# Kernel optimization log

Measured on AMD Instinct MI355X. Metric: run time of the kernel, lower is better.

Reference implementation:

```python
import jax, jax.numpy as jnp
import numpy as np

B, S, H, C = 2, 128, 768, 5
NEG = -1024.0

def setup_inputs() -> dict:
    key = jax.random.key(0)
    ks = jax.random.split(key, 6)
    sequence_output = jax.random.normal(ks[0], (B, S, H), dtype=jnp.float32)
    attention_mask = jnp.ones((B, S), dtype=jnp.int32)
    ng_token_mask = jax.random.bernoulli(ks[1], 0.5, (B, S, C, S))  # bool
    target = (jax.random.uniform(ks[2], (B, S, C, S)) < 0.01).astype(jnp.float32)
    lim = 1.0 / np.sqrt(H)
    W_prd = jax.random.uniform(ks[3], (H, H), jnp.float32, -lim, lim)
    b_prd = jnp.zeros((H,), jnp.float32)
    W_arg = jax.random.uniform(ks[4], (C * H, H), jnp.float32, -lim, lim)
    b_arg = jnp.zeros((C * H,), jnp.float32)
    W_out = jax.random.uniform(ks[5], (C, H), jnp.float32, -lim, lim)
    return dict(sequence_output=sequence_output, attention_mask=attention_mask,
                ng_token_mask=ng_token_mask, target=target,
                W_prd=W_prd, b_prd=b_prd, W_arg=W_arg, b_arg=b_arg, W_out=W_out)

def reference(sequence_output, attention_mask, ng_token_mask, target,
              W_prd, b_prd, W_arg, b_arg, W_out):
    b, s, h = sequence_output.shape
    c = W_out.shape[0]
    # get_mask: ng mask restricted to attended tokens, then any over case dim
    mask = ng_token_mask & (attention_mask[:, None, None, :] > 0)   # (B,S,C,S)
    mask = jnp.any(mask, axis=2, keepdims=True)                      # (B,S,1,S)
    # dropout is identity in eval mode
    h_p = sequence_output @ W_prd.T + b_prd                          # (B,S,H)
    h_a = (sequence_output @ W_arg.T + b_arg).reshape(b, s, c, h)    # (B,S,C,H)
    # outer-sum biaffine: (B, S_prd, S_arg, C, H)
    hh = jnp.tanh(h_p[:, :, None, None, :] + h_a[:, None, :, :, :])
    # per-case Linear(H,1,bias=False), stacked at dim=2 -> (B, S_prd, C, S_arg)
    output = jnp.einsum('bpach,ch->bpca', hh, W_out)
    output = output + (~mask).astype(output.dtype) * NEG
    # cross_entropy_pas_loss: multi-hot CE over candidate (last) axis
    log_sm = jax.nn.log_softmax(output, axis=3)
    loss = jnp.sum(-log_sm * target) / jnp.sum(target)
    return loss, output
```

## Files before the change

### kernel.cpp

```cpp
#include <hip/hip_runtime.h>
#include <math.h>

#define Bb 2
#define Ss 128
#define Hh 768
#define Cc 5
#define Mm 256
#define NEGV -1024.0f
#define SCALE 2.8853900817779268f

#define PT 2
#define NBLK (Mm / PT * Cc)
#define NBUCKET 32

typedef __attribute__((ext_vector_type(8))) short bf16x8;
typedef __attribute__((ext_vector_type(4))) float f32x4;
typedef unsigned short ushort;

__device__ __forceinline__ unsigned pack_hi16(float hi, float lo) {
    return (__float_as_uint(hi) & 0xFFFF0000u) | (__float_as_uint(lo) >> 16);
}
__device__ __forceinline__ bf16x8 pack_bf16x8(float4 lo, float4 hi) {
    union { bf16x8 v; unsigned u[4]; } r;
    r.u[0] = pack_hi16(lo.y, lo.x);
    r.u[1] = pack_hi16(lo.w, lo.z);
    r.u[2] = pack_hi16(hi.y, hi.x);
    r.u[3] = pack_hi16(hi.w, hi.z);
    return r.v;
}
__device__ __forceinline__ ushort bf16_rne(float f) {
    unsigned b = __float_as_uint(f);
    return (ushort)((b + 0x7FFFu + ((b >> 16) & 1u)) >> 16);
}

#define SB __builtin_amdgcn_sched_barrier(0);

__global__ __launch_bounds__(256)
void gemm_mfma(const float* __restrict__ X,
               const float* __restrict__ Wprd,
               const float* __restrict__ Warg,
               const float* __restrict__ bprd,
               const float* __restrict__ barg,
               float* __restrict__ EpG,
               ushort* __restrict__ haTb,
               float* __restrict__ accumArr)
{
    __shared__ __align__(16) ushort Asb[64][72];
    __shared__ __align__(16) ushort Bsb[32][72];

    if (blockIdx.x == 0 && blockIdx.y == 0) {
        for (int i = threadIdx.x; i < NBUCKET * 32; i += 256) accumArr[i] = 0.f;
    }
    const int bm   = blockIdx.x;
    const int bn   = blockIdx.y;
    const int tid  = threadIdx.x;
    const int wave = tid >> 6;
    const int lane = tid & 63;
    const int l16  = lane & 15;
    const int quad = lane >> 4;

    const float* Wsrc; const float* bsrc;
    const int nb = bn * 32;
    if (nb < Hh) { Wsrc = Wprd + (size_t)nb * Hh;        bsrc = bprd + nb; }
    else         { Wsrc = Warg + (size_t)(nb - Hh) * Hh; bsrc = barg + (nb - Hh); }

    const int srow = tid >> 2;
    const int sko  = (tid & 3) * 8;
    const float* gA = X + (size_t)(bm * 64 + srow) * Hh + sko;
    const float* gB = Wsrc + (size_t)(tid >> 2) * Hh + sko;

    float4 a00 = *(const float4*)(gA);
    float4 a01 = *(const float4*)(gA + 4);
    float4 a10 = *(const float4*)(gA + 32);
    float4 a11 = *(const float4*)(gA + 36);
    float4 b00, b01, b10, b11;
    if (tid < 128) {
        b00 = *(const float4*)(gB);      b01 = *(const float4*)(gB + 4);
        b10 = *(const float4*)(gB + 32); b11 = *(const float4*)(gB + 36);
    }

    f32x4 acc0 = {0.f,0.f,0.f,0.f}, acc1 = {0.f,0.f,0.f,0.f};

    for (int k0 = 0; k0 < Hh; k0 += 64) {
        *(bf16x8*)&Asb[srow][sko]      = pack_bf16x8(a00, a01);
        *(bf16x8*)&Asb[srow][sko + 32] = pack_bf16x8(a10, a11);
        if (tid < 128) {
            *(bf16x8*)&Bsb[tid >> 2][sko]      = pack_bf16x8(b00, b01);
            *(bf16x8*)&Bsb[tid >> 2][sko + 32] = pack_bf16x8(b10, b11);
        }
        __syncthreads();
        if (k0 + 64 < Hh) {
            a00 = *(const float4*)(gA + k0 + 64);
            a01 = *(const float4*)(gA + k0 + 68);
            a10 = *(const float4*)(gA + k0 + 96);
            a11 = *(const float4*)(gA + k0 + 100);
            if (tid < 128) {
                b00 = *(const float4*)(gB + k0 + 64);
                b01 = *(const float4*)(gB + k0 + 68);
                b10 = *(const float4*)(gB + k0 + 96);
                b11 = *(const float4*)(gB + k0 + 100);
            }
        }
        {
            bf16x8 af0 = *(const bf16x8*)&Asb[wave * 16 + l16][quad * 8];
            bf16x8 c00 = *(const bf16x8*)&Bsb[l16][quad * 8];
            bf16x8 c10 = *(const bf16x8*)&Bsb[16 + l16][quad * 8];
            acc0 = __builtin_amdgcn_mfma_f32_16x16x32_bf16(af0, c00, acc0, 0, 0, 0);
            acc1 = __builtin_amdgcn_mfma_f32_16x16x32_bf16(af0, c10, acc1, 0, 0, 0);
            bf16x8 af1 = *(const bf16x8*)&Asb[wave * 16 + l16][quad * 8 + 32];
            bf16x8 c01 = *(const bf16x8*)&Bsb[l16][quad * 8 + 32];
            bf16x8 c11 = *(const bf16x8*)&Bsb[16 + l16][quad * 8 + 32];
            acc0 = __builtin_amdgcn_mfma_f32_16x16x32_bf16(af1, c01, acc0, 0, 0, 0);
            acc1 = __builtin_amdgcn_mfma_f32_16x16x32_bf16(af1, c11, acc1, 0, 0, 0);
        }
        __syncthreads();
    }

    const float sb0 = SCALE * bsrc[l16];
    const float sb1 = SCALE * bsrc[16 + l16];
    const int row = bm * 64 + wave * 16 + quad * 4;

    if (nb < Hh) {
        #pragma unroll
        for (int r = 0; r < 4; ++r) {
            const int mm = row + r;
            EpG[(size_t)mm * Hh + nb + l16]      = __builtin_amdgcn_exp2f(SCALE * acc0[r] + sb0);
            EpG[(size_t)mm * Hh + nb + 16 + l16] = __builtin_amdgcn_exp2f(SCALE * acc1[r] + sb1);
        }
    } else {
        const int q  = nb - Hh;
        const int cU = q / Hh;
        const int h0 = q % Hh;
        const int hA = h0 + l16;
        const int hB = h0 + 16 + l16;
        const size_t offA = (size_t)(hA >> 3) * 1024 + (hA & 7);
        const size_t offB = (size_t)(hB >> 3) * 1024 + (hB & 7);
        #pragma unroll
        for (int r = 0; r < 4; ++r) {
            const int mm = row + r;
            const int bI = mm >> 7, aI = mm & 127;
            const size_t base = ((size_t)(bI * Cc + cU) * 96) * 1024 + (size_t)aI * 8;
            const float e0 = __builtin_amdgcn_exp2f(SCALE * acc0[r] + sb0);
            const float e1 = __builtin_amdgcn_exp2f(SCALE * acc1[r] + sb1);
            haTb[base + offA] = bf16_rne(e0);
            haTb[base + offB] = bf16_rne(e1);
        }
    }
}


#define LOADG4(R, g) \
    R##0 = hap4[(g)*256];       R##1 = hap4[(g)*256 + 64]; \
    R##2 = hap4[(g)*256 + 128]; R##3 = hap4[(g)*256 + 192];

#define TERM(ww, q0, q1, ea0, ea1, A00, A01, A10, A11) { \
    float r; \
    r = __builtin_amdgcn_rcpf(fmaf((q0), (ea0), 1.0f)); A00 = fmaf((ww), r, A00); \
    r = __builtin_amdgcn_rcpf(fmaf((q1), (ea0), 1.0f)); A10 = fmaf((ww), r, A10); \
    r = __builtin_amdgcn_rcpf(fmaf((q0), (ea1), 1.0f)); A01 = fmaf((ww), r, A01); \
    r = __builtin_amdgcn_rcpf(fmaf((q1), (ea1), 1.0f)); A11 = fmaf((ww), r, A11); \
}

#define C2(uA, uB, hx_) { \
    const int hx = (hx_); \
    const float4 w4a = *(const float4*)&wS[hx];      \
    const float4 w4b = *(const float4*)&wS[hx + 4];  \
    const float4 q04a = *(const float4*)&e0S[hx];    \
    const float4 q04b = *(const float4*)&e0S[hx + 4];\
    const float4 q14a = *(const float4*)&e1S[hx];    \
    const float4 q14b = *(const float4*)&e1S[hx + 4];\
    TERM(w4a.x, q04a.x, q14a.x, __uint_as_float((uA).x << 16),         __uint_as_float((uB).x << 16),         acE00, acE01, acE10, acE11) \
    TERM(w4a.y, q04a.y, q14a.y, __uint_as_float((uA).x & 0xFFFF0000u), __uint_as_float((uB).x & 0xFFFF0000u), acO00, acO01, acO10, acO11) \
    TERM(w4a.z, q04a.z, q14a.z, __uint_as_float((uA).y << 16),         __uint_as_float((uB).y << 16),         acE00, acE01, acE10, acE11) \
    TERM(w4a.w, q04a.w, q14a.w, __uint_as_float((uA).y & 0xFFFF0000u), __uint_as_float((uB).y & 0xFFFF0000u), acO00, acO01, acO10, acO11) \
    TERM(w4b.x, q04b.x, q14b.x, __uint_as_float((uA).z << 16),         __uint_as_float((uB).z << 16),         acE00, acE01, acE10, acE11) \
    TERM(w4b.y, q04b.y, q14b.y, __uint_as_float((uA).z & 0xFFFF0000u), __uint_as_float((uB).z & 0xFFFF0000u), acO00, acO01, acO10, acO11) \
    TERM(w4b.z, q04b.z, q14b.z, __uint_as_float((uA).w << 16),         __uint_as_float((uB).w << 16),         acE00, acE01, acE10, acE11) \
    TERM(w4b.w, q04b.w, q14b.w, __uint_as_float((uA).w & 0xFFFF0000u), __uint_as_float((uB).w & 0xFFFF0000u), acO00, acO01, acO10, acO11) \
}

#define CONSUMEG(R, g) \
    C2(R##0, R##1, hq96 + ((g)*2 + 0) * 8) \
    C2(R##2, R##3, hq96 + ((g)*2 + 1) * 8)

__global__ __launch_bounds__(512, 4)
void biaffine_loss(const float* __restrict__ EpG,
                   const ushort* __restrict__ haTb,
                   const float* __restrict__ Wout,
                   const int* __restrict__ ng,
                   const int* __restrict__ att,
                   const float* __restrict__ target,
                   float* __restrict__ out_logits,
                   float* __restrict__ accumArr)
{
    __shared__ float partial[PT][7][Ss];
    __shared__ float maskneg[PT][Ss];
    __shared__ float swr_s;
    __shared__ __align__(16) float wS[Hh];
    __shared__ __align__(16) float e0S[Hh];
    __shared__ __align__(16) float e1S[Hh];

    const int L   = ((int)blockIdx.x & 7) * 80 + ((int)blockIdx.x >> 3);
    const int g   = L >> 6;
    const int j   = L & 63;
    const int b   = (g >= Cc) ? 1 : 0;
    const int c   = g - b * Cc;
    const int bp0 = (b * 64 + j) * PT;
    const int tid  = threadIdx.x;
    const int lane = tid & 63;
    const int wvid = __builtin_amdgcn_readfirstlane(tid >> 6);
    const int hq96 = wvid * 96;

    const float* wrow = Wout + (size_t)c * Hh;
    const float* ep0  = EpG + (size_t)(bp0 + 0) * Hh;
    const float* ep1  = EpG + (size_t)(bp0 + 1) * Hh;

    if (tid < PT * Ss) {
        const int p_i = tid >> 7;
        const int aa  = tid & (Ss - 1);
        const int attv = att[b * Ss + aa];
        const int* ngp = ng + (size_t)(bp0 + p_i) * Cc * Ss + aa;
        const int n0 = ngp[0 * Ss], n1 = ngp[1 * Ss], n2 = ngp[2 * Ss],
                  n3 = ngp[3 * Ss], n4 = ngp[4 * Ss];
        const int any = (n0 | n1 | n2 | n3 | n4) & (attv > 0 ? -1 : 0);
        maskneg[p_i][aa] = any ? 0.0f : NEGV;
    }

    if (tid < 64) {
        float s = 0.f;
        #pragma unroll
        for (int i = 0; i < Hh / 64; ++i) s += wrow[tid + i * 64];
        #pragma unroll
        for (int off = 32; off; off >>= 1) s += __shfl_xor(s, off, 64);
        if (tid == 0) swr_s = s;
    }

    for (int i = tid; i < Hh; i += 512) {
        wS[i]  = wrow[i];
        e0S[i] = ep0[i];
        e1S[i] = ep1[i];
    }

    const uint4* hap4 = (const uint4*)(haTb + ((size_t)(b * Cc + c) * 96) * 1024)
                      + (size_t)wvid * 12 * 128 + lane;

    uint4 A0, A1, A2, A3;
    uint4 B0, B1, B2, B3;
    float acE00 = 0.f, acO00 = 0.f;
    float acE01 = 0.f, acO01 = 0.f;
    float acE10 = 0.f, acO10 = 0.f;
    float acE11 = 0.f, acO11 = 0.f;

    LOADG4(A, 0)
    LOADG4(B, 1)
    __syncthreads();
    CONSUMEG(A, 0)  LOADG4(A, 2)  SB
    CONSUMEG(B, 1)  LOADG4(B, 3)  SB
    CONSUMEG(A, 2)  LOADG4(A, 4)  SB
    CONSUMEG(B, 3)  LOADG4(B, 5)  SB
    CONSUMEG(A, 4)
    CONSUMEG(B, 5)

    if (wvid != 0) {
        partial[0][wvid - 1][lane]      = acE00 + acO00;
        partial[0][wvid - 1][lane + 64] = acE01 + acO01;
        partial[1][wvid - 1][lane]      = acE10 + acO10;
        partial[1][wvid - 1][lane + 64] = acE11 + acO11;
    }
    __syncthreads();

    if (wvid == 0) {
        float nsum = 0.f, dsum = 0.f;
        #pragma unroll
        for (int p = 0; p < PT; ++p) {
            float f0 = (p == 0) ? (acE00 + acO00) : (acE10 + acO10);
            float f1 = (p == 0) ? (acE01 + acO01) : (acE11 + acO11);
            #pragma unroll
            for (int k = 0; k < 7; ++k) {
                f0 += partial[p][k][lane];
                f1 += partial[p][k][lane + 64];
            }
            const float l0 = swr_s - 2.0f * f0 + maskneg[p][lane];
            const float l1 = swr_s - 2.0f * f1 + maskneg[p][lane + 64];
            const size_t obase = ((size_t)(bp0 + p) * Cc + c) * Ss;
            out_logits[obase + lane]      = l0;
            out_logits[obase + lane + 64] = l1;
            float mx = fmaxf(l0, l1);
            #pragma unroll
            for (int off = 32; off; off >>= 1) mx = fmaxf(mx, __shfl_xor(mx, off, 64));
            const float e = __builtin_amdgcn_exp2f((l0 - mx) * 1.4426950408889634f)
                          + __builtin_amdgcn_exp2f((l1 - mx) * 1.4426950408889634f);
            const float tg0 = target[obase + lane];
            const float tg1 = target[obase + lane + 64];
            float se = e, st = tg0 + tg1, sx = tg0 * l0 + tg1 * l1;
            #pragma unroll
            for (int off = 32; off; off >>= 1) {
                se += __shfl_xor(se, off, 64);
                st += __shfl_xor(st, off, 64);
                sx += __shfl_xor(sx, off, 64);
            }
            const float lse = mx + __builtin_amdgcn_logf(se) * 0.6931471805599453f;
            nsum += lse * st - sx;
            dsum += st;
        }
        if (lane == 0) {
            const int bkt = ((int)blockIdx.x & (NBUCKET - 1)) * 32;
            atomicAdd(&accumArr[bkt],     nsum);
            atomicAdd(&accumArr[bkt + 1], dsum);
        }
    }
}

__global__ __launch_bounds__(64)
void finalize_loss(const float* __restrict__ accumArr,
                   float* __restrict__ out_loss)
{
    const int lane = threadIdx.x;
    float n = 0.f, d = 0.f;
    if (lane < NBUCKET) { n = accumArr[lane * 32]; d = accumArr[lane * 32 + 1]; }
    #pragma unroll
    for (int off = 32; off; off >>= 1) {
        n += __shfl_xor(n, off, 64);
        d += __shfl_xor(d, off, 64);
    }
    if (lane == 0) out_loss[0] = n / d;
}

extern "C" void kernel_launch(void* const* d_in, const int* in_sizes, int n_in,
                              void* d_out, int out_size, void* d_ws, size_t ws_size,
                              hipStream_t stream) {
    const float* seq    = (const float*)d_in[0];
    const int*   att    = (const int*)  d_in[1];
    const int*   ng     = (const int*)  d_in[2];
    const float* target = (const float*)d_in[3];
    const float* Wprd   = (const float*)d_in[4];
    const float* bprd   = (const float*)d_in[5];
    const float* Warg   = (const float*)d_in[6];
    const float* barg   = (const float*)d_in[7];
    const float* Wout   = (const float*)d_in[8];

    float*  out      = (float*)d_out;
    float*  EpG      = (float*)d_ws;
    ushort* haTb     = (ushort*)(EpG + 196608);
    float*  accumArr = EpG + 196608 + 491520;

    gemm_mfma<<<dim3(4, 144), 256, 0, stream>>>(seq, Wprd, Warg, bprd, barg,
                                                EpG, haTb, accumArr);
    biaffine_loss<<<dim3(NBLK), 512, 0, stream>>>(EpG, haTb, Wout, ng, att, target,
                                                  out + 1, accumArr);
    finalize_loss<<<1, 64, 0, stream>>>(accumArr, out);
}
```

Measured before the change: 114.3 us.

## Overlap mask loads with main loop and split loss epilogue across two waves

The mask computation and the W_out row-sum move from before the first barrier to after the initial prefetch. The ng/att loads are issued into registers so they overlap the main accumulation, and the row-sum now reads shared memory instead of global. The epilogue now has every wave write its partial to shared memory, and two waves each handle one prd row's softmax and loss instead of one wave handling both serially. The GEMM grid axes are also swapped so consecutive blocks walk the N dimension. In exchange it adds more registers held across the main loop and more atomics.

Result: no change. 113.1 us, median of 2 (-1.0%).

```diff
diff --git a/kernel.cpp b/kernel.cpp
--- a/kernel.cpp
+++ b/kernel.cpp
@@ -51,8 +51,8 @@
     if (blockIdx.x == 0 && blockIdx.y == 0) {
         for (int i = threadIdx.x; i < NBUCKET * 32; i += 256) accumArr[i] = 0.f;
     }
-    const int bm   = blockIdx.x;
-    const int bn   = blockIdx.y;
+    const int bn   = blockIdx.x;
+    const int bm   = blockIdx.y;
     const int tid  = threadIdx.x;
     const int wave = tid >> 6;
     const int lane = tid & 63;
@@ -193,8 +193,7 @@
                    float* __restrict__ out_logits,
                    float* __restrict__ accumArr)
 {
-    __shared__ float partial[PT][7][Ss];
-    __shared__ float maskneg[PT][Ss];
+    __shared__ float partial[PT][8][Ss];
     __shared__ float swr_s;
     __shared__ __align__(16) float wS[Hh];
     __shared__ __align__(16) float e0S[Hh];
@@ -215,26 +214,6 @@
     const float* ep0  = EpG + (size_t)(bp0 + 0) * Hh;
     const float* ep1  = EpG + (size_t)(bp0 + 1) * Hh;
 
-    if (tid < PT * Ss) {
-        const int p_i = tid >> 7;
-        const int aa  = tid & (Ss - 1);
-        const int attv = att[b * Ss + aa];
-        const int* ngp = ng + (size_t)(bp0 + p_i) * Cc * Ss + aa;
-        const int n0 = ngp[0 * Ss], n1 = ngp[1 * Ss], n2 = ngp[2 * Ss],
-                  n3 = ngp[3 * Ss], n4 = ngp[4 * Ss];
-        const int any = (n0 | n1 | n2 | n3 | n4) & (attv > 0 ? -1 : 0);
-        maskneg[p_i][aa] = any ? 0.0f : NEGV;
-    }
-
-    if (tid < 64) {
-        float s = 0.f;
-        #pragma unroll
-        for (int i = 0; i < Hh / 64; ++i) s += wrow[tid + i * 64];
-        #pragma unroll
-        for (int off = 32; off; off >>= 1) s += __shfl_xor(s, off, 64);
-        if (tid == 0) swr_s = s;
-    }
-
     for (int i = tid; i < Hh; i += 512) {
         wS[i]  = wrow[i];
         e0S[i] = ep0[i];
@@ -254,6 +233,30 @@
     LOADG4(A, 0)
     LOADG4(B, 1)
     __syncthreads();
+
+    int attv0 = 0, attv1 = 0;
+    int ngA0 = 0, ngA1 = 0, ngA2 = 0, ngA3 = 0, ngA4 = 0;
+    int ngB0 = 0, ngB1 = 0, ngB2 = 0, ngB3 = 0, ngB4 = 0;
+    if (wvid < 2) {
+        attv0 = att[b * Ss + lane];
+        attv1 = att[b * Ss + lane + 64];
+        const int* ngp = ng + (size_t)(bp0 + wvid) * Cc * Ss;
+        ngA0 = ngp[0*Ss + lane];      ngB0 = ngp[0*Ss + lane + 64];
+        ngA1 = ngp[1*Ss + lane];      ngB1 = ngp[1*Ss + lane + 64];
+        ngA2 = ngp[2*Ss + lane];      ngB2 = ngp[2*Ss + lane + 64];
+        ngA3 = ngp[3*Ss + lane];      ngB3 = ngp[3*Ss + lane + 64];
+        ngA4 = ngp[4*Ss + lane];      ngB4 = ngp[4*Ss + lane + 64];
+    }
+    if (wvid == 2) {
+        float s = 0.f;
+        #pragma unroll
+        for (int i = 0; i < Hh / 64; ++i) s += wS[lane + i * 64];
+        #pragma unroll
+        for (int off = 32; off; off >>= 1) s += __shfl_xor(s, off, 64);
+        if (lane == 0) swr_s = s;
+    }
+    SB
+
     CONSUMEG(A, 0)  LOADG4(A, 2)  SB
     CONSUMEG(B, 1)  LOADG4(B, 3)  SB
     CONSUMEG(A, 2)  LOADG4(A, 4)  SB
@@ -261,52 +264,48 @@
     CONSUMEG(A, 4)
     CONSUMEG(B, 5)
 
-    if (wvid != 0) {
-        partial[0][wvid - 1][lane]      = acE00 + acO00;
-        partial[0][wvid - 1][lane + 64] = acE01 + acO01;
-        partial[1][wvid - 1][lane]      = acE10 + acO10;
-        partial[1][wvid - 1][lane + 64] = acE11 + acO11;
-    }
+    partial[0][wvid][lane]      = acE00 + acO00;
+    partial[0][wvid][lane + 64] = acE01 + acO01;
+    partial[1][wvid][lane]      = acE10 + acO10;
+    partial[1][wvid][lane + 64] = acE11 + acO11;
     __syncthreads();
 
-    if (wvid == 0) {
-        float nsum = 0.f, dsum = 0.f;
-        #pragma unroll
-        for (int p = 0; p < PT; ++p) {
-            float f0 = (p == 0) ? (acE00 + acO00) : (acE10 + acO10);
-            float f1 = (p == 0) ? (acE01 + acO01) : (acE11 + acO11);
-            #pragma unroll
-            for (int k = 0; k < 7; ++k) {
-                f0 += partial[p][k][lane];
-                f1 += partial[p][k][lane + 64];
-            }
-            const float l0 = swr_s - 2.0f * f0 + maskneg[p][lane];
-            const float l1 = swr_s - 2.0f * f1 + maskneg[p][lane + 64];
-            const size_t obase = ((size_t)(bp0 + p) * Cc + c) * Ss;
-            out_logits[obase + lane]      = l0;
-            out_logits[obase + lane + 64] = l1;
-            float mx = fmaxf(l0, l1);
-            #pragma unroll
-            for (int off = 32; off; off >>= 1) mx = fmaxf(mx, __shfl_xor(mx, off, 64));
-            const float e = __builtin_amdgcn_exp2f((l0 - mx) * 1.4426950408889634f)
-                          + __builtin_amdgcn_exp2f((l1 - mx) * 1.4426950408889634f);
-            const float tg0 = target[obase + lane];
-            const float tg1 = target[obase + lane + 64];
-            float se = e, st = tg0 + tg1, sx = tg0 * l0 + tg1 * l1;
-            #pragma unroll
-            for (int off = 32; off; off >>= 1) {
-                se += __shfl_xor(se, off, 64);
-                st += __shfl_xor(st, off, 64);
-                sx += __shfl_xor(sx, off, 64);
-            }
-            const float lse = mx + __builtin_amdgcn_logf(se) * 0.6931471805599453f;
-            nsum += lse * st - sx;
-            dsum += st;
-        }
+    if (wvid < 2) {
+        const int p = wvid;
+        const size_t obase = ((size_t)(bp0 + p) * Cc + c) * Ss;
+        const float tg0 = target[obase + lane];
+        const float tg1 = target[obase + lane + 64];
+        float f0 = 0.f, f1 = 0.f;
+        #pragma unroll
+        for (int k = 0; k < 8; ++k) {
+            f0 += partial[p][k][lane];
+            f1 += partial[p][k][lane + 64];
+        }
+        const int any0 = (ngA0 | ngA1 | ngA2 | ngA3 | ngA4) & (attv0 > 0 ? -1 : 0);
+        const int any1 = (ngB0 | ngB1 | ngB2 | ngB3 | ngB4) & (attv1 > 0 ? -1 : 0);
+        const float mk0 = any0 ? 0.0f : NEGV;
+        const float mk1 = any1 ? 0.0f : NEGV;
+        const float l0 = swr_s - 2.0f * f0 + mk0;
+        const float l1 = swr_s - 2.0f * f1 + mk1;
+        out_logits[obase + lane]      = l0;
+        out_logits[obase + lane + 64] = l1;
+        float mx = fmaxf(l0, l1);
+        #pragma unroll
+        for (int off = 32; off; off >>= 1) mx = fmaxf(mx, __shfl_xor(mx, off, 64));
+        const float e = __builtin_amdgcn_exp2f((l0 - mx) * 1.4426950408889634f)
+                      + __builtin_amdgcn_exp2f((l1 - mx) * 1.4426950408889634f);
+        float se = e, st = tg0 + tg1, sx = tg0 * l0 + tg1 * l1;
+        #pragma unroll
+        for (int off = 32; off; off >>= 1) {
+            se += __shfl_xor(se, off, 64);
+            st += __shfl_xor(st, off, 64);
+            sx += __shfl_xor(sx, off, 64);
+        }
+        const float lse = mx + __builtin_amdgcn_logf(se) * 0.6931471805599453f;
         if (lane == 0) {
             const int bkt = ((int)blockIdx.x & (NBUCKET - 1)) * 32;
-            atomicAdd(&accumArr[bkt],     nsum);
-            atomicAdd(&accumArr[bkt + 1], dsum);
+            atomicAdd(&accumArr[bkt],     lse * st - sx);
+            atomicAdd(&accumArr[bkt + 1], st);
         }
     }
 }
@@ -344,7 +343,7 @@
     ushort* haTb     = (ushort*)(EpG + 196608);
     float*  accumArr = EpG + 196608 + 491520;
 
-    gemm_mfma<<<dim3(4, 144), 256, 0, stream>>>(seq, Wprd, Warg, bprd, barg,
+    gemm_mfma<<<dim3(144, 4), 256, 0, stream>>>(seq, Wprd, Warg, bprd, barg,
                                                 EpG, haTb, accumArr);
     biaffine_loss<<<dim3(NBLK), 512, 0, stream>>>(EpG, haTb, Wout, ng, att, target,
                                                   out + 1, accumArr);
```
